# Optimization experiments

Measured on AMD Instinct MI355X. Metric: run time of the kernel, lower is better.

Reference implementation:

```python
import jax, jax.numpy as jnp
import numpy as np

B, C, N, H = 4, 256, 2048, 8
D = C // 4  # q/k projection dim
BN_EPS = 1e-5


def setup_inputs() -> dict:
    key = jax.random.key(0)
    ks = jax.random.split(key, 16)
    s = lambda fan: 1.0 / np.sqrt(fan)
    return {
        "x": jax.random.normal(ks[0], (B, C, N), dtype=jnp.float32),
        # per-head params, stacked on leading head axis
        "w_qk": jax.random.normal(ks[1], (H, D, C), dtype=jnp.float32) * s(C),  # shared q/k conv weight
        "w_v": jax.random.normal(ks[2], (H, C, C), dtype=jnp.float32) * s(C),
        "b_v": jax.random.normal(ks[3], (H, C), dtype=jnp.float32) * 0.01,
        "w_t": jax.random.normal(ks[4], (H, C, C), dtype=jnp.float32) * s(C),
        "b_t": jax.random.normal(ks[5], (H, C), dtype=jnp.float32) * 0.01,
        "bn_g": jnp.ones((H, C), dtype=jnp.float32),
        "bn_b": jnp.zeros((H, C), dtype=jnp.float32),
        "bn_m": jax.random.normal(ks[6], (H, C), dtype=jnp.float32) * 0.1,
        "bn_v": jax.random.uniform(ks[7], (H, C), dtype=jnp.float32, minval=0.5, maxval=1.5),
        # final 1x1 conv + BN (LeakyReLU 0.2)
        "w_lin": jax.random.normal(ks[8], (C, C * H), dtype=jnp.float32) * s(C * H),
        "lbn_g": jnp.ones((C,), dtype=jnp.float32),
        "lbn_b": jnp.zeros((C,), dtype=jnp.float32),
        "lbn_m": jax.random.normal(ks[9], (C,), dtype=jnp.float32) * 0.1,
        "lbn_v": jax.random.uniform(ks[10], (C,), dtype=jnp.float32, minval=0.5, maxval=1.5),
    }


def _oa_head(x, w_qk, w_v, b_v, w_t, b_t, g, b, m, v):
    # x: [B, C, N]; 1x1 Conv1d == channel matmul
    x_q = jnp.einsum("dc,bcn->bnd", w_qk, x)                 # [B, N, D]
    x_k = jnp.einsum("dc,bcn->bdn", w_qk, x)                 # [B, D, N] (shared weight)
    x_v = jnp.einsum("ec,bcn->ben", w_v, x) + b_v[:, None]   # [B, C, N]
    energy = jnp.einsum("bnd,bdm->bnm", x_q, x_k)            # [B, N, N]
    attn = jax.nn.softmax(energy, axis=-1)
    attn = attn / (1e-9 + attn.sum(axis=1, keepdims=True))   # extra L1 renorm over dim=1
    x_r = jnp.einsum("ben,bnm->bem", x_v, attn)              # [B, C, N]
    y = jnp.einsum("ec,bcn->ben", w_t, x - x_r) + b_t[:, None]
    y = (y - m[:, None]) * (g[:, None] / jnp.sqrt(v[:, None] + BN_EPS)) + b[:, None]
    return x + jax.nn.relu(y)


def reference(x, w_qk, w_v, b_v, w_t, b_t, bn_g, bn_b, bn_m, bn_v,
              w_lin, lbn_g, lbn_b, lbn_m, lbn_v):
    # run all H heads via vmap over stacked params -> [B, H, C, N]
    heads = jax.vmap(_oa_head, in_axes=(None, 0, 0, 0, 0, 0, 0, 0, 0, 0), out_axes=1)(
        x, w_qk, w_v, b_v, w_t, b_t, bn_g, bn_b, bn_m, bn_v)
    cat = heads.reshape(x.shape[0], H * C, x.shape[2])       # torch.cat(dim=1) order
    y = jnp.einsum("ck,bkn->bcn", w_lin, cat)                # 1x1 conv, no bias
    y = (y - lbn_m[:, None]) * (lbn_g[:, None] / jnp.sqrt(lbn_v[:, None] + BN_EPS)) + lbn_b[:, None]
    return jnp.where(y >= 0, y, 0.2 * y)                     # LeakyReLU(0.2)
```

## Files before the change

### kernel.cpp

```cpp
#include <hip/hip_runtime.h>
#include <math.h>

#define B_ 4
#define C_ 256
#define N_ 2048
#define H_ 8
#define D_ 64
#define BH_ 32
#define HC_ 2048
#define BN_EPS 1e-5f
#define SCL 1.2011224087864498f

typedef __attribute__((ext_vector_type(8))) short s8v;
typedef __attribute__((ext_vector_type(4))) short s4v;
typedef __attribute__((ext_vector_type(8))) _Float16 h8v;
typedef __attribute__((ext_vector_type(4))) _Float16 h4v;
typedef __attribute__((ext_vector_type(4))) float f32x4;

#define MFMA __builtin_amdgcn_mfma_f32_16x16x32_bf16
#define MFMAH __builtin_amdgcn_mfma_f32_16x16x32_f16

static __device__ __forceinline__ unsigned short f2b(float f) {
  union { float f; unsigned int i; } v; v.f = f;
  unsigned int r = v.i + 0x7FFFu + ((v.i >> 16) & 1u);
  return (unsigned short)(r >> 16);
}
static __device__ __forceinline__ float fexp2(float x) {
  float r;
  asm("v_exp_f32 %0, %1" : "=v"(r) : "v"(x));
  return r;
}
static __device__ __forceinline__ unsigned cvtpk(float lo, float hi) {
  unsigned r;
  asm("v_cvt_pk_bf16_f32 %0, %1, %2" : "=v"(r) : "v"(lo), "v"(hi));
  return r;
}
static __device__ __forceinline__ void gload16(const void* g, void* l) {
  __builtin_amdgcn_global_load_lds(
      (const __attribute__((address_space(1))) unsigned int*)g,
      (__attribute__((address_space(3))) unsigned int*)l, 16, 0, 0);
}

struct GP {
  const float *x, *w_qk, *w_v, *b_v, *w_t, *b_t, *bn_g, *bn_b, *bn_m, *bn_v;
  const float *w_lin, *lbn_g, *lbn_b, *lbn_m, *lbn_v;
  _Float16 *PT, *xT, *wqk16, *wvh;
  short *HOT, *wtb, *wlinb, *Vb, *xmr;
  float *part, *shb, *nrm, *sh, *out;
};

__global__ __launch_bounds__(256) void prep_k(GP p) {
  int u = blockIdx.x * 256 + threadIdx.x;
  if (u < 131072) {
    int i = u * 4;
    float4 v = *(const float4*)(p.w_t + i);
    s4v o = { (short)f2b(v.x), (short)f2b(v.y), (short)f2b(v.z), (short)f2b(v.w) };
    *(s4v*)(p.wtb + i) = o;
  } else if (u < 262144) {
    int i = (u - 131072) * 4;
    float4 v = *(const float4*)(p.w_lin + i);
    s4v o = { (short)f2b(v.x), (short)f2b(v.y), (short)f2b(v.z), (short)f2b(v.w) };
    *(s4v*)(p.wlinb + i) = o;
  } else if (u < 393216) {
    int i = (u - 262144) * 4;
    float4 v = *(const float4*)(p.w_v + i);
    h4v o = { (_Float16)v.x, (_Float16)v.y, (_Float16)v.z, (_Float16)v.w };
    *(h4v*)(p.wvh + i) = o;
  } else {
    int i = (u - 393216) * 4;
    float4 v = *(const float4*)(p.w_qk + i);
    h4v o = { (_Float16)v.x, (_Float16)v.y, (_Float16)v.z, (_Float16)v.w };
    *(h4v*)(p.wqk16 + i) = o;
  }
}

__global__ __launch_bounds__(256) void xcvt_k(const float* __restrict__ x,
                                              _Float16* __restrict__ xT) {
  const int n0 = blockIdx.x * 64, c0 = blockIdx.y * 64, b = blockIdx.z;
  const float* xb = x + (size_t)b * C_ * N_;
  __shared__ float sm[64][65];
  const int t = threadIdx.x;
#pragma unroll
  for (int i = 0; i < 4; ++i) {
    int idx = i * 256 + t;
    int c = idx >> 4, j = (idx & 15) * 4;
    float4 v = *(const float4*)(xb + (size_t)(c0 + c) * N_ + n0 + j);
    sm[j + 0][c] = v.x; sm[j + 1][c] = v.y; sm[j + 2][c] = v.z; sm[j + 3][c] = v.w;
  }
  __syncthreads();
#pragma unroll
  for (int i = 0; i < 2; ++i) {
    int idx = i * 256 + t;
    int n = idx >> 3, cg = (idx & 7) * 8;
    h8v o;
#pragma unroll
    for (int d = 0; d < 8; ++d) o[d] = (_Float16)sm[n][cg + d];
    *(h8v*)(xT + ((size_t)b * N_ + n0 + n) * C_ + c0 + cg) = o;
  }
}

__global__ __launch_bounds__(256, 2) void p_k(GP p) {
  const int t = threadIdx.x, wv = t >> 6, lane = t & 63;
  const int l15 = lane & 15, l4 = lane >> 4;
  const int n0 = blockIdx.x * 128;
  const int bh = blockIdx.y, b = bh / H_, h = bh % H_;
  const _Float16* Ag = p.wqk16 + h * D_ * C_;
  const _Float16* Bg = p.xT + (size_t)b * N_ * C_;
  __shared__ _Float16 As[64 * 64], Bs[128 * 64];
  __shared__ float Tr[128 * 65];
  f32x4 acc[4][2] = {};
  for (int kc = 0; kc < 256; kc += 64) {
    __syncthreads();
#pragma unroll
    for (int i = 0; i < 2; ++i) {
      int idx = i * 256 + t;
      int row = idx >> 3, offl = (idx & 7) * 16;
      gload16((const char*)(Ag + (size_t)row * C_ + kc) + (offl ^ ((row & 7) << 4)),
              (char*)As + idx * 16);
    }
#pragma unroll
    for (int i = 0; i < 4; ++i) {
      int idx = i * 256 + t;
      int row = idx >> 3, offl = (idx & 7) * 16;
      gload16((const char*)(Bg + (size_t)(n0 + row) * C_ + kc) + (offl ^ ((row & 7) << 4)),
              (char*)Bs + idx * 16);
    }
    __syncthreads();
    h8v ad[4][2], bn[2][2];
#pragma unroll
    for (int d = 0; d < 4; ++d)
#pragma unroll
      for (int ks = 0; ks < 2; ++ks) {
        int row = d * 16 + l15;
        ad[d][ks] = *(const h8v*)((const char*)As + row * 128 + ((ks * 64 + l4 * 16) ^ ((row & 7) << 4)));
      }
#pragma unroll
    for (int nb = 0; nb < 2; ++nb)
#pragma unroll
      for (int ks = 0; ks < 2; ++ks) {
        int row = wv * 32 + nb * 16 + l15;
        bn[nb][ks] = *(const h8v*)((const char*)Bs + row * 128 + ((ks * 64 + l4 * 16) ^ ((row & 7) << 4)));
      }
#pragma unroll
    for (int d = 0; d < 4; ++d)
#pragma unroll
      for (int nb = 0; nb < 2; ++nb) {
        acc[d][nb] = MFMAH(ad[d][0], bn[nb][0], acc[d][nb], 0, 0, 0);
        acc[d][nb] = MFMAH(ad[d][1], bn[nb][1], acc[d][nb], 0, 0, 0);
      }
  }
  __syncthreads();
#pragma unroll
  for (int d = 0; d < 4; ++d)
#pragma unroll
    for (int nb = 0; nb < 2; ++nb)
#pragma unroll
      for (int r = 0; r < 4; ++r) {
        int n_l = wv * 32 + nb * 16 + l15;
        int dd = d * 16 + l4 * 4 + r;
        Tr[n_l * 65 + dd] = acc[d][nb][r];
      }
  __syncthreads();
  _Float16* Pf = p.PT + ((size_t)bh * N_ + n0) * D_;
  float* nz = p.nrm + (size_t)bh * N_;
#pragma unroll
  for (int i = 0; i < 4; ++i) {
    int idx = i * 256 + t;
    int n = idx >> 3, dg = (idx & 7) * 8;
    h8v hv;
    float ssq = 0.f;
#pragma unroll
    for (int j = 0; j < 8; ++j) {
      float v = Tr[n * 65 + dg + j] * SCL;
      ssq = fmaf(v, v, ssq);
      hv[j] = (_Float16)v;
    }
    *(h8v*)(Pf + (size_t)n * D_ + dg) = hv;
    ssq += __shfl_xor(ssq, 1, 64);
    ssq += __shfl_xor(ssq, 2, 64);
    ssq += __shfl_xor(ssq, 4, 64);
    if ((t & 7) == 0) nz[n0 + n] = ssq;
  }
}

__global__ __launch_bounds__(256) void shift_k(const float* __restrict__ nrm,
                                               float* __restrict__ sh) {
  const int z = blockIdx.x, t = threadIdx.x;
  const float* nz = nrm + (size_t)z * N_;
  float loc[8];
  float mx = 0.f;
#pragma unroll
  for (int i = 0; i < 8; ++i) {
    loc[i] = nz[i * 256 + t];
    mx = fmaxf(mx, loc[i]);
  }
  for (int o = 32; o; o >>= 1) mx = fmaxf(mx, __shfl_xor(mx, o, 64));
  __shared__ float sb[4];
  if ((t & 63) == 0) sb[t >> 6] = mx;
  __syncthreads();
  float M = sqrtf(fmaxf(fmaxf(sb[0], sb[1]), fmaxf(sb[2], sb[3])));
#pragma unroll
  for (int i = 0; i < 8; ++i)
    sh[(size_t)z * N_ + i * 256 + t] = sqrtf(loc[i]) * M;
}

__global__ __launch_bounds__(256, 4) void passa_k(GP p) {
  const int t = threadIdx.x, wv = t >> 6, lane = t & 63;
  const int l15 = lane & 15, l4 = lane >> 4;
  const int wr = wv >> 1, wc = wv & 1;
  const int z = blockIdx.x;
  int idx = blockIdx.y;
  int ti = 0;
  while (idx >= 16 - ti) { idx -= 16 - ti; ++ti; }
  const int tj = ti + idx;
  const int r0 = ti * 128, c0 = tj * 128;
  const _Float16* Pz = p.PT + (size_t)z * N_ * D_;
  const float* shz = p.sh + (size_t)z * N_;
  __shared__ short RH[8192], CH[8192];
  __shared__ float rbuf[2][2][64], cbuf[2][2][64];
#pragma unroll
  for (int i = 0; i < 4; ++i) {
    int c2 = i * 256 + t;
    int row = c2 >> 3, offl = (c2 & 7) * 16;
    int so = offl ^ ((row & 7) << 4);
    gload16((const char*)(Pz + (size_t)(r0 + row) * D_) + so, (char*)RH + c2 * 16);
    if (ti != tj)
      gload16((const char*)(Pz + (size_t)(c0 + row) * D_) + so, (char*)CH + c2 * 16);
  }
  __syncthreads();
  const char* BHp = (ti == tj) ? (const char*)RH : (const char*)CH;

  h8v bh4[4][2];
  float shc[4];
#pragma unroll
  for (int nf = 0; nf < 4; ++nf) {
#pragma unroll
    for (int ks = 0; ks < 2; ++ks) {
      int row = wc * 64 + nf * 16 + l15;
      int byte = row * 128 + ((ks * 64 + l4 * 16) ^ ((row & 7) << 4));
      bh4[nf][ks] = *(const h8v*)(BHp + byte);
    }
    shc[nf] = shz[c0 + wc * 64 + nf * 16 + l15];
  }
  float rowp[4][4] = {};
  float colp[4] = {};
#pragma unroll
  for (int mf = 0; mf < 4; ++mf) {
    h8v ah[2];
#pragma unroll
    for (int ks = 0; ks < 2; ++ks) {
      int row = wr * 64 + mf * 16 + l15;
      int byte = row * 128 + ((ks * 64 + l4 * 16) ^ ((row & 7) << 4));
      ah[ks] = *(const h8v*)((const char*)RH + byte);
    }
    f32x4 shr = *(const f32x4*)(shz + r0 + wr * 64 + mf * 16 + l4 * 4);
#pragma unroll
    for (int nf = 0; nf < 4; ++nf) {
      f32x4 s = {};
      s = MFMAH(ah[0], bh4[nf][0], s, 0, 0, 0);
      s = MFMAH(ah[1], bh4[nf][1], s, 0, 0, 0);
      rowp[mf][0] += fexp2(s[0] - shr[0]);
      rowp[mf][1] += fexp2(s[1] - shr[1]);
      rowp[mf][2] += fexp2(s[2] - shr[2]);
      rowp[mf][3] += fexp2(s[3] - shr[3]);
      if (ti != tj)
        colp[nf] += fexp2(s[0] - shc[nf]) + fexp2(s[1] - shc[nf]) +
                    fexp2(s[2] - shc[nf]) + fexp2(s[3] - shc[nf]);
    }
  }
#pragma unroll
  for (int mf = 0; mf < 4; ++mf)
#pragma unroll
    for (int r = 0; r < 4; ++r) {
      float v = rowp[mf][r];
      v += __shfl_xor(v, 1, 64); v += __shfl_xor(v, 2, 64);
      v += __shfl_xor(v, 4, 64); v += __shfl_xor(v, 8, 64);
      rowp[mf][r] = v;
    }
#pragma unroll
  for (int nf = 0; nf < 4; ++nf) {
    float v = colp[nf];
    v += __shfl_xor(v, 16, 64); v += __shfl_xor(v, 32, 64);
    colp[nf] = v;
  }
  if (l15 == 0)
#pragma unroll
    for (int mf = 0; mf < 4; ++mf)
#pragma unroll
      for (int r = 0; r < 4; ++r)
        rbuf[wr][wc][mf * 16 + l4 * 4 + r] = rowp[mf][r];
  if (l4 == 0)
#pragma unroll
    for (int nf = 0; nf < 4; ++nf)
      cbuf[wc][wr][nf * 16 + l15] = colp[nf];
  __syncthreads();
  if (t < 128) {
    float v = rbuf[t >> 6][0][t & 63] + rbuf[t >> 6][1][t & 63];
    p.part[((size_t)z * 16 + tj) * N_ + r0 + t] = v;
  } else if (ti != tj) {
    int u = t - 128;
    float v = cbuf[u >> 6][0][u & 63] + cbuf[u >> 6][1][u & 63];
    p.part[((size_t)z * 16 + ti) * N_ + c0 + u] = v;
  }
}

__global__ __launch_bounds__(256) void shbred_k(const float* __restrict__ part,
                                                const float* __restrict__ sh,
                                                float* __restrict__ shb) {
  int i = blockIdx.x * 256 + threadIdx.x;
  int z = i >> 11, n = i & 2047;
  const float* pz = part + ((size_t)z * 16) * N_ + n;
  float s = 0.f;
#pragma unroll
  for (int j = 0; j < 16; ++j) s += pz[(size_t)j * N_];
  shb[i] = sh[i] + __log2f(s);
}

__global__ __launch_bounds__(256, 2) void passb_k(GP p) {
  const int t = threadIdx.x, wv = t >> 6, lane = t & 63;
  const int l15 = lane & 15, l4 = lane >> 4;
  const int z = blockIdx.x, b = z / H_;
  const int m0 = blockIdx.y * 128;
  const _Float16* Pz = p.PT + (size_t)z * N_ * D_;
  const short* Vz = p.Vb + (size_t)z * C_ * N_;
  const float* shbz = p.shb + (size_t)z * N_;

  __shared__ char smem[57856];
  float* cs_sm = (float*)(smem + 49152);
  float* shs = (float*)(smem + 49664);

  h8v bm[2][2];
#pragma unroll
  for (int mf = 0; mf < 2; ++mf)
#pragma unroll
    for (int ks = 0; ks < 2; ++ks)
      bm[mf][ks] = *(const h8v*)(Pz + (size_t)(m0 + wv * 32 + mf * 16 + l15) * D_ + ks * 32 + l4 * 8);

  s8v va[4][2];

#define STAGE_PN(n0v, bufbyte) do { \
    _Pragma("unroll") \
    for (int i_ = 0; i_ < 2; ++i_) { \
      int sl_ = i_ * 256 + t; \
      int rw_ = sl_ >> 3, of_ = (sl_ & 7) * 16; \
      gload16((const char*)(Pz + (size_t)((n0v) + rw_) * D_) + (of_ ^ ((rw_ & 7) << 4)), \
              smem + (bufbyte) + sl_ * 16); \
    } \
  } while (0)
#define ISSUE_V(n0v) do { \
    _Pragma("unroll") \
    for (int eb = 0; eb < 4; ++eb) { \
      const short* vr_ = Vz + (size_t)(wv * 64 + eb * 16 + l15) * N_ + (n0v) + l4 * 8; \
      va[eb][0] = *(const s8v*)vr_; \
      va[eb][1] = *(const s8v*)(vr_ + 32); \
    } \
  } while (0)

  f32x4 racc[4][8] = {};
  float csa0 = 0.f, csa1 = 0.f;

  STAGE_PN(0, 0);
  STAGE_PN(64, 8192);
  ISSUE_V(0);
#pragma unroll
  for (int i = 0; i < 2; ++i) {
    int ii = i * 256 + t;
    *(float4*)(shs + ii * 4) = *(const float4*)(shbz + ii * 4);
  }
  __syncthreads();

  for (int it = 0; it < 32; ++it) {
    const int n0 = it * 64;
    const int cur = it & 1;
    const char* PH = smem + cur * 8192;
    char* AT = smem + 16384 + cur * 16384;
#pragma unroll
    for (int nb = 0; nb < 4; ++nb) {
      int rowb = nb * 16 + l15;
      int sw = (rowb & 7) << 4;
      h8v an0 = *(const h8v*)(PH + rowb * 128 + ((l4 * 16) ^ sw));
      h8v an1 = *(const h8v*)(PH + rowb * 128 + ((64 + l4 * 16) ^ sw));
      f32x4 s0 = {}, s1 = {};
      s0 = MFMAH(an0, bm[0][0], s0, 0, 0, 0);
      s0 = MFMAH(an1, bm[0][1], s0, 0, 0, 0);
      s1 = MFMAH(an0, bm[1][0], s1, 0, 0, 0);
      s1 = MFMAH(an1, bm[1][1], s1, 0, 0, 0);
      f32x4 sb4 = *(const f32x4*)(shs + n0 + nb * 16 + l4 * 4);
      float a0 = fexp2(s0[0] - sb4[0]);
      float a1 = fexp2(s0[1] - sb4[1]);
      float a2 = fexp2(s0[2] - sb4[2]);
      float a3 = fexp2(s0[3] - sb4[3]);
      float c0 = fexp2(s1[0] - sb4[0]);
      float c1 = fexp2(s1[1] - sb4[1]);
      float c2 = fexp2(s1[2] - sb4[2]);
      float c3 = fexp2(s1[3] - sb4[3]);
      csa0 += (a0 + a1) + (a2 + a3);
      csa1 += (c0 + c1) + (c2 + c3);
      uint2 pk0 = { cvtpk(a0, a1), cvtpk(a2, a3) };
      uint2 pk1 = { cvtpk(c0, c1), cvtpk(c2, c3) };
      int swm = (l15 & 7) << 4;
      int cb = (nb * 32 + l4 * 8);
      *(uint2*)(AT + (wv * 32 + l15) * 128 + (cb ^ swm)) = pk0;
      *(uint2*)(AT + (wv * 32 + 16 + l15) * 128 + (cb ^ swm)) = pk1;
    }
    asm volatile("s_waitcnt vmcnt(8) lgkmcnt(0)" ::: "memory");
    __builtin_amdgcn_s_barrier();
    __builtin_amdgcn_sched_barrier(0);
    if (it < 30) STAGE_PN(n0 + 128, cur * 8192);
    __builtin_amdgcn_s_setprio(1);
#pragma unroll
    for (int mb = 0; mb < 8; ++mb) {
      int rowb = mb * 16 + l15;
      int sw = (rowb & 7) << 4;
      s8v at0 = *(const s8v*)(AT + rowb * 128 + ((l4 * 16) ^ sw));
      s8v at1 = *(const s8v*)(AT + rowb * 128 + ((64 + l4 * 16) ^ sw));
#pragma unroll
      for (int eb = 0; eb < 4; ++eb) {
        racc[eb][mb] = MFMA(va[eb][0], at0, racc[eb][mb], 0, 0, 0);
        racc[eb][mb] = MFMA(va[eb][1], at1, racc[eb][mb], 0, 0, 0);
      }
    }
    __builtin_amdgcn_s_setprio(0);
    if (it < 31) ISSUE_V(n0 + 64);
  }

  csa0 += __shfl_xor(csa0, 16, 64);
  csa0 += __shfl_xor(csa0, 32, 64);
  csa1 += __shfl_xor(csa1, 16, 64);
  csa1 += __shfl_xor(csa1, 32, 64);
  if (l4 == 0) {
    cs_sm[wv * 32 + l15] = csa0;
    cs_sm[wv * 32 + 16 + l15] = csa1;
  }
  __syncthreads();
  float invc[8];
#pragma unroll
  for (int mb = 0; mb < 8; ++mb) invc[mb] = 1.0f / (1e-9f + cs_sm[mb * 16 + l15]);
  const float* xb = p.x + (size_t)b * C_ * N_;
  char* Tr = smem;
#pragma unroll
  for (int half = 0; half < 2; ++half) {
    if (half) __syncthreads();
#pragma unroll
    for (int eb = 0; eb < 4; ++eb)
#pragma unroll
      for (int mbh = 0; mbh < 4; ++mbh) {
        int mb = half * 4 + mbh;
        int e0 = wv * 64 + eb * 16 + l4 * 4;
        int m_l = mbh * 16 + l15;
        int mg = m0 + mb * 16 + l15;
        float v0 = xb[(size_t)(e0 + 0) * N_ + mg] - racc[eb][mb][0] * invc[mb];
        float v1 = xb[(size_t)(e0 + 1) * N_ + mg] - racc[eb][mb][1] * invc[mb];
        float v2 = xb[(size_t)(e0 + 2) * N_ + mg] - racc[eb][mb][2] * invc[mb];
        float v3 = xb[(size_t)(e0 + 3) * N_ + mg] - racc[eb][mb][3] * invc[mb];
        uint2 pk = { cvtpk(v0, v1), cvtpk(v2, v3) };
        *(uint2*)(Tr + m_l * 512 + ((e0 * 2) ^ ((m_l & 7) << 4))) = pk;
      }
    __syncthreads();
    short* xz = p.xmr + ((size_t)z * N_ + m0 + half * 64) * C_;
#pragma unroll
    for (int i = 0; i < 8; ++i) {
      int idx = i * 256 + t;
      int m_l = idx >> 5, off2 = (idx & 31) * 16;
      s8v v = *(const s8v*)(Tr + m_l * 512 + (off2 ^ ((m_l & 7) << 4)));
      *(s8v*)((char*)(xz + (size_t)m_l * C_) + off2) = v;
    }
  }
#undef STAGE_PN
#undef ISSUE_V
}

template<int EPI>
__global__ __launch_bounds__(256) void mm_k(GP p) {
  constexpr int K = 256;
  const int t = threadIdx.x;
  const int wave = t >> 6, lane = t & 63;
  const int wr = wave >> 1, wc = wave & 1;
  const int l15 = lane & 15, l4 = lane >> 4;
  const int n0 = blockIdx.x * 128;
  const int m0 = blockIdx.y * 128;
  const int z = blockIdx.z;
  int b = z / H_, h = z % H_;

  const short *Ag, *Bg;
  if constexpr (EPI == 1) {
    Ag = (const short*)(p.wvh + (size_t)h * C_ * C_);
    Bg = (const short*)(p.xT + (size_t)b * N_ * C_);
  } else {
    Ag = p.wtb + (size_t)h * C_ * C_;
    Bg = p.xmr + (size_t)z * N_ * C_;
  }

  __shared__ short As[128 * 32];
  __shared__ short Bs[128 * 32];

  f32x4 acc[4][4] = {};

  for (int k0 = 0; k0 < K; k0 += 32) {
    __syncthreads();
#pragma unroll
    for (int i = 0; i < 2; ++i) {
      int idx = i * 256 + t;
      int row = idx >> 2, kg = (idx & 3) * 8;
      gload16(Ag + (size_t)(m0 + row) * K + k0 + kg, (char*)As + idx * 16);
      gload16(Bg + (size_t)(n0 + row) * K + k0 + kg, (char*)Bs + idx * 16);
    }
    __syncthreads();
    s8v af[4], bf[4];
#pragma unroll
    for (int m = 0; m < 4; ++m) af[m] = *(const s8v*)&As[(wr * 64 + m * 16 + l15) * 32 + l4 * 8];
#pragma unroll
    for (int n = 0; n < 4; ++n) bf[n] = *(const s8v*)&Bs[(wc * 64 + n * 16 + l15) * 32 + l4 * 8];
#pragma unroll
    for (int m = 0; m < 4; ++m)
#pragma unroll
      for (int n = 0; n < 4; ++n) {
        if constexpr (EPI == 1)
          acc[m][n] = MFMAH(__builtin_bit_cast(h8v, af[m]), __builtin_bit_cast(h8v, bf[n]),
                            acc[m][n], 0, 0, 0);
        else
          acc[m][n] = MFMA(af[m], bf[n], acc[m][n], 0, 0, 0);
      }
  }

  if constexpr (EPI == 1) {
    short* Vz = p.Vb + (size_t)z * C_ * N_;
#pragma unroll
    for (int m = 0; m < 4; ++m)
#pragma unroll
      for (int r = 0; r < 4; ++r) {
        int e = m0 + wr * 64 + m * 16 + l4 * 4 + r;
        float bias = p.b_v[h * C_ + e];
#pragma unroll
        for (int n = 0; n < 4; ++n) {
          int c = n0 + wc * 64 + n * 16 + l15;
          Vz[(size_t)e * N_ + c] = (short)f2b(acc[m][n][r] + bias);
        }
      }
  } else {
    __shared__ short Tr[128 * 128];
    const float* xb = p.x + (size_t)b * C_ * N_;
#pragma unroll
    for (int m = 0; m < 4; ++m)
#pragma unroll
      for (int r = 0; r < 4; ++r) {
        int e = m0 + wr * 64 + m * 16 + l4 * 4 + r;
        int el = e - m0;
        int hc = h * C_ + e;
        float bt = p.b_t[hc], mm = p.bn_m[hc], bb = p.bn_b[hc];
        float sc = p.bn_g[hc] / sqrtf(p.bn_v[hc] + BN_EPS);
#pragma unroll
        for (int n = 0; n < 4; ++n) {
          int cl = wc * 64 + n * 16 + l15;
          float y = (acc[m][n][r] + bt - mm) * sc + bb;
          float val = xb[(size_t)e * N_ + n0 + cl] + fmaxf(y, 0.f);
          Tr[cl * 128 + el] = (short)f2b(val);
        }
      }
    __syncthreads();
    short* Hz = p.HOT + (size_t)b * N_ * HC_;
#pragma unroll
    for (int it = 0; it < 8; ++it) {
      int idx = it * 256 + t;
      int cl = idx >> 4, eg = (idx & 15) * 8;
      *(s8v*)(Hz + (size_t)(n0 + cl) * HC_ + h * C_ + m0 + eg) = *(const s8v*)&Tr[cl * 128 + eg];
    }
  }
}

__global__ __launch_bounds__(256, 2) void mm4_k(GP p) {
  const int t = threadIdx.x, wv = t >> 6, lane = t & 63;
  const int l15 = lane & 15, l4 = lane >> 4;
  const int n0 = blockIdx.x * 128;
  const int m0 = blockIdx.y * 64;
  const int b = blockIdx.z;
  const short* Ag = p.wlinb;
  const short* Bg = p.HOT + (size_t)b * N_ * HC_;
  __shared__ short As[64 * 64], Bs[128 * 64];
  f32x4 acc[4][2] = {};
  for (int k0 = 0; k0 < HC_; k0 += 64) {
    __syncthreads();
#pragma unroll
    for (int i = 0; i < 2; ++i) {
      int sl = i * 256 + t;
      int rw = sl >> 3, of = (sl & 7) * 16;
      gload16((const char*)(Ag + (size_t)(m0 + rw) * HC_ + k0) + (of ^ ((rw & 7) << 4)),
              (char*)As + sl * 16);
    }
#pragma unroll
    for (int i = 0; i < 4; ++i) {
      int sl = i * 256 + t;
      int rw = sl >> 3, of = (sl & 7) * 16;
      gload16((const char*)(Bg + (size_t)(n0 + rw) * HC_ + k0) + (of ^ ((rw & 7) << 4)),
              (char*)Bs + sl * 16);
    }
    __syncthreads();
    s8v af[4][2], bf[2][2];
#pragma unroll
    for (int m = 0; m < 4; ++m)
#pragma unroll
      for (int ks = 0; ks < 2; ++ks) {
        int rw = m * 16 + l15;
        af[m][ks] = *(const s8v*)((const char*)As + rw * 128 + ((ks * 64 + l4 * 16) ^ ((rw & 7) << 4)));
      }
#pragma unroll
    for (int nf = 0; nf < 2; ++nf)
#pragma unroll
      for (int ks = 0; ks < 2; ++ks) {
        int rw = wv * 32 + nf * 16 + l15;
        bf[nf][ks] = *(const s8v*)((const char*)Bs + rw * 128 + ((ks * 64 + l4 * 16) ^ ((rw & 7) << 4)));
      }
#pragma unroll
    for (int m = 0; m < 4; ++m)
#pragma unroll
      for (int nf = 0; nf < 2; ++nf) {
        acc[m][nf] = MFMA(af[m][0], bf[nf][0], acc[m][nf], 0, 0, 0);
        acc[m][nf] = MFMA(af[m][1], bf[nf][1], acc[m][nf], 0, 0, 0);
      }
  }
  float* ob = p.out + (size_t)b * C_ * N_;
#pragma unroll
  for (int m = 0; m < 4; ++m)
#pragma unroll
    for (int r = 0; r < 4; ++r) {
      int e = m0 + m * 16 + l4 * 4 + r;
      float mm = p.lbn_m[e], bb = p.lbn_b[e];
      float sc = p.lbn_g[e] / sqrtf(p.lbn_v[e] + BN_EPS);
#pragma unroll
      for (int nf = 0; nf < 2; ++nf) {
        int c = n0 + wv * 32 + nf * 16 + l15;
        float y = (acc[m][nf][r] - mm) * sc + bb;
        ob[(size_t)e * N_ + c] = y >= 0.f ? y : 0.2f * y;
      }
    }
}

extern "C" void kernel_launch(void* const* d_in, const int* in_sizes, int n_in,
                              void* d_out, int out_size, void* d_ws, size_t ws_size,
                              hipStream_t stream) {
  GP p;
  p.x     = (const float*)d_in[0];
  p.w_qk  = (const float*)d_in[1];
  p.w_v   = (const float*)d_in[2];
  p.b_v   = (const float*)d_in[3];
  p.w_t   = (const float*)d_in[4];
  p.b_t   = (const float*)d_in[5];
  p.bn_g  = (const float*)d_in[6];
  p.bn_b  = (const float*)d_in[7];
  p.bn_m  = (const float*)d_in[8];
  p.bn_v  = (const float*)d_in[9];
  p.w_lin = (const float*)d_in[10];
  p.lbn_g = (const float*)d_in[11];
  p.lbn_b = (const float*)d_in[12];
  p.lbn_m = (const float*)d_in[13];
  p.lbn_v = (const float*)d_in[14];
  p.out   = (float*)d_out;

  char* base = (char*)d_ws;
  size_t off = 0;
  auto alloc = [&](size_t bytes) -> char* {
    char* r = base + off;
    off += (bytes + 255) & ~(size_t)255;
    return r;
  };
  p.PT    = (_Float16*)alloc((size_t)BH_ * N_ * D_ * 2);
  p.xT    = (_Float16*)alloc((size_t)B_ * N_ * C_ * 2);
  p.wqk16 = (_Float16*)alloc((size_t)H_ * D_ * C_ * 2);
  p.wvh   = (_Float16*)alloc((size_t)H_ * C_ * C_ * 2);
  p.wtb   = (short*)alloc((size_t)H_ * C_ * C_ * 2);
  p.wlinb = (short*)alloc((size_t)C_ * HC_ * 2);
  p.Vb    = (short*)alloc((size_t)BH_ * C_ * N_ * 2);
  p.xmr   = (short*)alloc((size_t)BH_ * N_ * C_ * 2);
  p.part  = (float*)alloc((size_t)BH_ * 16 * N_ * 4);
  p.shb   = (float*)alloc((size_t)BH_ * N_ * 4);
  p.nrm   = (float*)alloc((size_t)BH_ * N_ * 4);
  p.sh    = (float*)alloc((size_t)BH_ * N_ * 4);
  p.HOT   = p.Vb;

  dim3 blk(256);

  prep_k<<<1664, blk, 0, stream>>>(p);
  xcvt_k<<<dim3(32, 4, B_), blk, 0, stream>>>(p.x, p.xT);
  p_k<<<dim3(16, BH_), blk, 0, stream>>>(p);
  shift_k<<<BH_, blk, 0, stream>>>(p.nrm, p.sh);
  mm_k<1><<<dim3(16, 2, BH_), blk, 0, stream>>>(p);
  passa_k<<<dim3(32, 136), blk, 0, stream>>>(p);
  shbred_k<<<256, blk, 0, stream>>>(p.part, p.sh, p.shb);
  passb_k<<<dim3(32, 16), blk, 0, stream>>>(p);
  mm_k<3><<<dim3(16, 2, BH_), blk, 0, stream>>>(p);
  mm4_k<<<dim3(16, 4, B_), blk, 0, stream>>>(p);
}
```

Measured before the change: 220.2 us.

## Software-pipeline attention loop so PV of one tile overlaps QK of next

The attention main loop is restructured so that each iteration runs the P·V MFMAs for tile `it` and then the QK/exp/softmax-numerator phase for tile `it+1`, with a single barrier per iteration. The QK phase of tile 0 becomes a prologue and the PV phase of tile 31 an epilogue. The aim is to let the scheduler interleave the exp and pack VALU work with the bf16 MFMA stream, instead of separating them across a barrier. The V register loads for the next tile are now issued later, after both phases, which may expose more load latency. Register pressure may also rise.

```diff
diff --git a/kernel.cpp b/kernel.cpp
--- a/kernel.cpp
+++ b/kernel.cpp
@@ -337,6 +337,8 @@
       bm[mf][ks] = *(const h8v*)(Pz + (size_t)(m0 + wv * 32 + mf * 16 + l15) * D_ + ks * 32 + l4 * 8);
 
   s8v va[4][2];
+  f32x4 racc[4][8] = {};
+  float csa0 = 0.f, csa1 = 0.f;
 
 #define STAGE_PN(n0v, bufbyte) do { \
     _Pragma("unroll") \
@@ -355,9 +357,60 @@
       va[eb][1] = *(const s8v*)(vr_ + 32); \
     } \
   } while (0)
-
-  f32x4 racc[4][8] = {};
-  float csa0 = 0.f, csa1 = 0.f;
+#define QK_PHASE(jj) do { \
+    const int n0_ = (jj) * 64; \
+    const char* PH_ = smem + ((jj) & 1) * 8192; \
+    char* AT_ = smem + 16384 + ((jj) & 1) * 16384; \
+    _Pragma("unroll") \
+    for (int nb = 0; nb < 4; ++nb) { \
+      int rowb = nb * 16 + l15; \
+      int sw = (rowb & 7) << 4; \
+      h8v an0 = *(const h8v*)(PH_ + rowb * 128 + ((l4 * 16) ^ sw)); \
+      h8v an1 = *(const h8v*)(PH_ + rowb * 128 + ((64 + l4 * 16) ^ sw)); \
+      f32x4 s0 = {}, s1 = {}; \
+      s0 = MFMAH(an0, bm[0][0], s0, 0, 0, 0); \
+      s0 = MFMAH(an1, bm[0][1], s0, 0, 0, 0); \
+      s1 = MFMAH(an0, bm[1][0], s1, 0, 0, 0); \
+      s1 = MFMAH(an1, bm[1][1], s1, 0, 0, 0); \
+      f32x4 sb4 = *(const f32x4*)(shs + n0_ + nb * 16 + l4 * 4); \
+      float a0 = fexp2(s0[0] - sb4[0]); \
+      float a1 = fexp2(s0[1] - sb4[1]); \
+      float a2 = fexp2(s0[2] - sb4[2]); \
+      float a3 = fexp2(s0[3] - sb4[3]); \
+      float c0 = fexp2(s1[0] - sb4[0]); \
+      float c1 = fexp2(s1[1] - sb4[1]); \
+      float c2 = fexp2(s1[2] - sb4[2]); \
+      float c3 = fexp2(s1[3] - sb4[3]); \
+      csa0 += (a0 + a1) + (a2 + a3); \
+      csa1 += (c0 + c1) + (c2 + c3); \
+      uint2 pk0 = { cvtpk(a0, a1), cvtpk(a2, a3) }; \
+      uint2 pk1 = { cvtpk(c0, c1), cvtpk(c2, c3) }; \
+      int swm = (l15 & 7) << 4; \
+      int cb = (nb * 32 + l4 * 8); \
+      *(uint2*)(AT_ + (wv * 32 + l15) * 128 + (cb ^ swm)) = pk0; \
+      *(uint2*)(AT_ + (wv * 32 + 16 + l15) * 128 + (cb ^ swm)) = pk1; \
+    } \
+  } while (0)
+#define PV_PHASE(jj) do { \
+    char* AT_ = smem + 16384 + ((jj) & 1) * 16384; \
+    _Pragma("unroll") \
+    for (int mb = 0; mb < 8; ++mb) { \
+      int rowb = mb * 16 + l15; \
+      int sw = (rowb & 7) << 4; \
+      s8v at0 = *(const s8v*)(AT_ + rowb * 128 + ((l4 * 16) ^ sw)); \
+      s8v at1 = *(const s8v*)(AT_ + rowb * 128 + ((64 + l4 * 16) ^ sw)); \
+      _Pragma("unroll") \
+      for (int eb = 0; eb < 4; ++eb) { \
+        racc[eb][mb] = MFMA(va[eb][0], at0, racc[eb][mb], 0, 0, 0); \
+        racc[eb][mb] = MFMA(va[eb][1], at1, racc[eb][mb], 0, 0, 0); \
+      } \
+    } \
+  } while (0)
+#define FENCE() do { \
+    asm volatile("s_waitcnt vmcnt(8) lgkmcnt(0)" ::: "memory"); \
+    __builtin_amdgcn_s_barrier(); \
+    __builtin_amdgcn_sched_barrier(0); \
+  } while (0)
 
   STAGE_PN(0, 0);
   STAGE_PN(64, 8192);
@@ -368,61 +421,19 @@
     *(float4*)(shs + ii * 4) = *(const float4*)(shbz + ii * 4);
   }
   __syncthreads();
-
-  for (int it = 0; it < 32; ++it) {
-    const int n0 = it * 64;
-    const int cur = it & 1;
-    const char* PH = smem + cur * 8192;
-    char* AT = smem + 16384 + cur * 16384;
-#pragma unroll
-    for (int nb = 0; nb < 4; ++nb) {
-      int rowb = nb * 16 + l15;
-      int sw = (rowb & 7) << 4;
-      h8v an0 = *(const h8v*)(PH + rowb * 128 + ((l4 * 16) ^ sw));
-      h8v an1 = *(const h8v*)(PH + rowb * 128 + ((64 + l4 * 16) ^ sw));
-      f32x4 s0 = {}, s1 = {};
-      s0 = MFMAH(an0, bm[0][0], s0, 0, 0, 0);
-      s0 = MFMAH(an1, bm[0][1], s0, 0, 0, 0);
-      s1 = MFMAH(an0, bm[1][0], s1, 0, 0, 0);
-      s1 = MFMAH(an1, bm[1][1], s1, 0, 0, 0);
-      f32x4 sb4 = *(const f32x4*)(shs + n0 + nb * 16 + l4 * 4);
-      float a0 = fexp2(s0[0] - sb4[0]);
-      float a1 = fexp2(s0[1] - sb4[1]);
-      float a2 = fexp2(s0[2] - sb4[2]);
-      float a3 = fexp2(s0[3] - sb4[3]);
-      float c0 = fexp2(s1[0] - sb4[0]);
-      float c1 = fexp2(s1[1] - sb4[1]);
-      float c2 = fexp2(s1[2] - sb4[2]);
-      float c3 = fexp2(s1[3] - sb4[3]);
-      csa0 += (a0 + a1) + (a2 + a3);
-      csa1 += (c0 + c1) + (c2 + c3);
-      uint2 pk0 = { cvtpk(a0, a1), cvtpk(a2, a3) };
-      uint2 pk1 = { cvtpk(c0, c1), cvtpk(c2, c3) };
-      int swm = (l15 & 7) << 4;
-      int cb = (nb * 32 + l4 * 8);
-      *(uint2*)(AT + (wv * 32 + l15) * 128 + (cb ^ swm)) = pk0;
-      *(uint2*)(AT + (wv * 32 + 16 + l15) * 128 + (cb ^ swm)) = pk1;
-    }
-    asm volatile("s_waitcnt vmcnt(8) lgkmcnt(0)" ::: "memory");
-    __builtin_amdgcn_s_barrier();
-    __builtin_amdgcn_sched_barrier(0);
-    if (it < 30) STAGE_PN(n0 + 128, cur * 8192);
+  QK_PHASE(0);
+  FENCE();
+
+  for (int it = 0; it < 31; ++it) {
+    if (it < 30) STAGE_PN((it + 2) * 64, (it & 1) * 8192);
     __builtin_amdgcn_s_setprio(1);
-#pragma unroll
-    for (int mb = 0; mb < 8; ++mb) {
-      int rowb = mb * 16 + l15;
-      int sw = (rowb & 7) << 4;
-      s8v at0 = *(const s8v*)(AT + rowb * 128 + ((l4 * 16) ^ sw));
-      s8v at1 = *(const s8v*)(AT + rowb * 128 + ((64 + l4 * 16) ^ sw));
-#pragma unroll
-      for (int eb = 0; eb < 4; ++eb) {
-        racc[eb][mb] = MFMA(va[eb][0], at0, racc[eb][mb], 0, 0, 0);
-        racc[eb][mb] = MFMA(va[eb][1], at1, racc[eb][mb], 0, 0, 0);
-      }
-    }
+    PV_PHASE(it);
+    QK_PHASE(it + 1);
     __builtin_amdgcn_s_setprio(0);
-    if (it < 31) ISSUE_V(n0 + 64);
-  }
+    ISSUE_V((it + 1) * 64);
+    FENCE();
+  }
+  PV_PHASE(31);
 
   csa0 += __shfl_xor(csa0, 16, 64);
   csa0 += __shfl_xor(csa0, 32, 64);
@@ -468,6 +479,9 @@
   }
 #undef STAGE_PN
 #undef ISSUE_V
+#undef QK_PHASE
+#undef PV_PHASE
+#undef FENCE
 }
 
 template<int EPI>
```

Measured after the change: 224.2 us. About the same (+1.8%).
